# Kernel optimization log

Hardware: AMD Instinct MI355X
Metric: run time of the kernel (lower is better)

The kernel has to match this reference:

```python
import jax, jax.numpy as jnp
import numpy as np
from jax import lax

DIM = 512; NUM_HEADS = 8; WS = 2; POOL = 3
HEAD_DIM = DIM // NUM_HEADS
L_HEADS = int(NUM_HEADS * 0.5); L_DIM = L_HEADS * HEAD_DIM
H_HEADS = NUM_HEADS - L_HEADS; H_DIM = H_HEADS * HEAD_DIM
SCALE = HEAD_DIM ** (-0.5)


def setup_inputs():
    key = jax.random.key(0)
    ks = jax.random.split(key, 8)
    B, Hh, Ww = 8, 64, 64
    N = Hh * Ww
    s = lambda fan: 1.0 / np.sqrt(fan)
    return {
        'x': jax.random.normal(ks[0], (B, N, DIM), jnp.float32),
        'H': Hh,
        'l_q_w': jax.random.normal(ks[1], (DIM, L_DIM), jnp.float32) * s(DIM),
        'l_kv_w': jax.random.normal(ks[2], (DIM, 2 * L_DIM), jnp.float32) * s(DIM),
        'l_proj_w': jax.random.normal(ks[3], (L_DIM, L_DIM), jnp.float32) * s(L_DIM),
        'l_proj_b': jax.random.normal(ks[4], (L_DIM,), jnp.float32) * 0.01,
        'h_qkv_w': jax.random.normal(ks[5], (DIM, H_DIM), jnp.float32) * s(DIM),
        'h_proj_w': jax.random.normal(ks[6], (H_DIM, H_DIM), jnp.float32) * s(H_DIM),
        'h_proj_b': jax.random.normal(ks[7], (H_DIM,), jnp.float32) * 0.01,
    }


def _avgpool3_same(x):
    # x: [M, ws, ws, C]; 3x3 avg pool, stride 1, pad 1, count_include_pad=False
    ssum = lax.reduce_window(x, jnp.float32(0.0), lax.add,
                             (1, POOL, POOL, 1), (1, 1, 1, 1),
                             ((0, 0), (1, 1), (1, 1), (0, 0)))
    ones = jnp.ones(x.shape[1:3], x.dtype)
    cnt = lax.reduce_window(ones, jnp.float32(0.0), lax.add,
                            (POOL, POOL), (1, 1), ((1, 1), (1, 1)))
    return ssum / cnt[None, :, :, None]


def _hifi(x, h_qkv_w, h_proj_w, h_proj_b):
    B, H, W, C = x.shape
    hg, wg = H // WS, W // WS
    x = x @ h_qkv_w  # [B,H,W,H_DIM]
    # partition into ws x ws windows: [B*hg*wg, ws, ws, H_DIM]
    xw = x.reshape(B, hg, WS, wg, WS, H_DIM).transpose(0, 1, 3, 2, 4, 5)
    xw = xw.reshape(B * hg * wg, WS, WS, H_DIM)
    xw = _avgpool3_same(xw) - xw
    xw = xw.reshape(B, hg, wg, WS, WS, H_DIM).transpose(0, 1, 3, 2, 4, 5)
    xw = xw.reshape(B, H, W, H_DIM)
    return xw @ h_proj_w + h_proj_b


def _lofi(x, l_q_w, l_kv_w, l_proj_w, l_proj_b):
    B, H, W, C = x.shape
    q = (x @ l_q_w).reshape(B, H * W, L_HEADS, HEAD_DIM).transpose(0, 2, 1, 3)
    # spatial reduction: avg pool ws stride ws -> [B, H/ws * W/ws, C]
    xp = x.reshape(B, H // WS, WS, W // WS, WS, C).mean(axis=(2, 4))
    xp = xp.reshape(B, -1, C)
    kv = (xp @ l_kv_w).reshape(B, -1, 2, L_HEADS, HEAD_DIM)
    k = kv[:, :, 0].transpose(0, 2, 1, 3)  # [B,h,M,d]
    v = kv[:, :, 1].transpose(0, 2, 1, 3)
    attn = jax.nn.softmax(jnp.einsum('bhnd,bhmd->bhnm', q, k) * SCALE, axis=-1)
    out = jnp.einsum('bhnm,bhmd->bhnd', attn, v)
    out = out.transpose(0, 2, 1, 3).reshape(B, H, W, L_DIM)
    return out @ l_proj_w + l_proj_b


def reference(x, H, l_q_w, l_kv_w, l_proj_w, l_proj_b, h_qkv_w, h_proj_w, h_proj_b):
    B, N, C = x.shape
    W = N // H
    xg = x.reshape(B, H, W, C)
    hi = _hifi(xg, h_qkv_w, h_proj_w, h_proj_b)
    lo = _lofi(xg, l_q_w, l_kv_w, l_proj_w, l_proj_b)
    out = jnp.concatenate([hi, lo], axis=-1)  # [B,H,W,C]
    return out.reshape(B, N, C)
```

## Files before the change

### kernel.cpp

```cpp
#include <hip/hip_runtime.h>

typedef __bf16 bf16x8 __attribute__((ext_vector_type(8)));
typedef float  f32x4  __attribute__((ext_vector_type(4)));
typedef unsigned int u32x4 __attribute__((ext_vector_type(4)));
typedef unsigned short u16x8 __attribute__((ext_vector_type(8)));
typedef unsigned short u16x4 __attribute__((ext_vector_type(4)));
typedef short i16x4 __attribute__((ext_vector_type(4)));

__device__ __forceinline__ unsigned short f2bf(float f) {
    return __builtin_bit_cast(unsigned short, (__bf16)f);
}
__device__ __forceinline__ float bf2f(unsigned short s) {
    return (float)__builtin_bit_cast(__bf16, s);
}
__device__ __forceinline__ bf16x8 as_bf16x8(u32x4 v) {
    return __builtin_bit_cast(bf16x8, v);
}

#define AS1 __attribute__((address_space(1)))
#define AS3 __attribute__((address_space(3)))
__device__ __forceinline__ void gload_lds16(const void* g, void* l) {
    __builtin_amdgcn_global_load_lds((const AS1 void*)g, (AS3 void*)l, 16, 0, 0);
}


__global__ __launch_bounds__(256) void k_prep(
        const float* __restrict__ x,
        const float* __restrict__ h_qkv_w, const float* __restrict__ l_q_w,
        const float* __restrict__ l_kv_w, const float* __restrict__ h_proj_w,
        const float* __restrict__ l_proj_w,
        unsigned short* __restrict__ xb, unsigned short* __restrict__ xpb,
        unsigned short* __restrict__ wcatT, unsigned short* __restrict__ lkvT,
        unsigned short* __restrict__ hprojT, unsigned short* __restrict__ lprojT) {
    int blk = blockIdx.x;
    if (blk < 8192) {
        int t = blk * 256 + threadIdx.x;
        int row = t >> 6, c8 = (t & 63) << 3;
        int b = row >> 12, nn = row & 4095;
        int hh = nn >> 6, ww = nn & 63;
        int mp = (((b << 10) + ((hh >> 1) << 5) + (ww >> 1)) << 2) + ((hh & 1) << 1) + (ww & 1);
        const float* src = x + (size_t)row * 512 + c8;
        f32x4 v0 = *(const f32x4*)src;
        f32x4 v1 = *(const f32x4*)(src + 4);
        u16x8 o = { f2bf(v0[0]), f2bf(v0[1]), f2bf(v0[2]), f2bf(v0[3]),
                    f2bf(v1[0]), f2bf(v1[1]), f2bf(v1[2]), f2bf(v1[3]) };
        *(u16x8*)(xb + (size_t)mp * 512 + c8) = o;
    } else if (blk < 10240) {
        int t = (blk - 8192) * 256 + threadIdx.x;
        int r = t >> 6, c8 = (t & 63) << 3;
        int b = r >> 10, hw = r & 1023;
        int h2 = hw >> 5, w2 = hw & 31;
        const float* base = x + ((size_t)(b << 12) + (h2 << 7) + (w2 << 1)) * 512 + c8;
        u16x8 o;
#pragma unroll
        for (int half = 0; half < 2; half++) {
            f32x4 a0 = *(const f32x4*)(base + half * 4);
            f32x4 a1 = *(const f32x4*)(base + 512 + half * 4);
            f32x4 a2 = *(const f32x4*)(base + 64 * 512 + half * 4);
            f32x4 a3 = *(const f32x4*)(base + 65 * 512 + half * 4);
            f32x4 m = (a0 + a1 + a2 + a3) * 0.25f;
#pragma unroll
            for (int j = 0; j < 4; j++) o[half * 4 + j] = f2bf(m[j]);
        }
        *(u16x8*)(xpb + (size_t)r * 512 + c8) = o;
    } else {
        int i = (blk - 10240) * 256 + threadIdx.x;
        if (i < 262144) {
            int n = i >> 9, k = i & 511;
            float v = (n < 256) ? h_qkv_w[k * 256 + n] : l_q_w[k * 256 + (n - 256)];
            wcatT[i] = f2bf(v);
        } else if (i < 524288) {
            int j = i - 262144; int n = j >> 9, k = j & 511;
            lkvT[j] = f2bf(l_kv_w[k * 512 + n]);
        } else if (i < 589824) {
            int j = i - 524288; int n = j >> 8, k = j & 255;
            hprojT[j] = f2bf(h_proj_w[k * 256 + n]);
        } else {
            int j = i - 589824; int n = j >> 8, k = j & 255;
            lprojT[j] = f2bf(l_proj_w[k * 256 + n]);
        }
    }
}

__device__ __forceinline__ void mm_core(
        const unsigned short* __restrict__ A, const unsigned short* __restrict__ Bt,
        size_t row0, int col0, int K,
        unsigned short* As, unsigned short* Bs, f32x4 (&acc)[4][4]) {
    const int tid = threadIdx.x;
    const int wave = tid >> 6, lane = tid & 63;
    const int m16 = lane & 15, quad = lane >> 4;
    const int wr = wave >> 1, wc = wave & 1;
    const int srow = lane >> 2;
    const int scol = (lane & 3) * 8;
    const unsigned short* Ap0 = A + (row0 + wave * 32 + srow) * (size_t)K + scol;
    const unsigned short* Ap1 = Ap0 + (size_t)16 * K;
    const unsigned short* Bp0 = Bt + (size_t)(col0 + wave * 32 + srow) * K + scol;
    const unsigned short* Bp1 = Bp0 + (size_t)16 * K;
    unsigned short* Al0 = As + wave * 1024;
    unsigned short* Al1 = As + wave * 1024 + 512;
    unsigned short* Bl0 = Bs + wave * 1024;
    unsigned short* Bl1 = Bs + wave * 1024 + 512;

    for (int k0 = 0; k0 < K; k0 += 32) {
        __syncthreads();
        gload_lds16(Ap0 + k0, Al0);
        gload_lds16(Ap1 + k0, Al1);
        gload_lds16(Bp0 + k0, Bl0);
        gload_lds16(Bp1 + k0, Bl1);
        __syncthreads();
        bf16x8 af[4], bfr[4];
#pragma unroll
        for (int mi = 0; mi < 4; mi++)
            af[mi] = as_bf16x8(*(const u32x4*)(As + (wr * 64 + mi * 16 + m16) * 32 + quad * 8));
#pragma unroll
        for (int ni = 0; ni < 4; ni++)
            bfr[ni] = as_bf16x8(*(const u32x4*)(Bs + (wc * 64 + ni * 16 + m16) * 32 + quad * 8));
#pragma unroll
        for (int mi = 0; mi < 4; mi++)
#pragma unroll
            for (int ni = 0; ni < 4; ni++)
                acc[mi][ni] = __builtin_amdgcn_mfma_f32_16x16x32_bf16(af[mi], bfr[ni], acc[mi][ni], 0, 0, 0);
    }
}

__global__ __launch_bounds__(256, 2) void k_mm512(
        const unsigned short* __restrict__ xb, const unsigned short* __restrict__ xpb,
        const unsigned short* __restrict__ wcatT, const unsigned short* __restrict__ lkvT,
        unsigned short* __restrict__ dbuf, unsigned short* __restrict__ qbuf,
        unsigned short* __restrict__ kbuf, unsigned short* __restrict__ vT) {
    __shared__ __align__(16) unsigned short As[128 * 32];
    __shared__ __align__(16) unsigned short Bs[128 * 32];
    const int flat = blockIdx.x;
    const bool isg1 = flat < 1024;
    const unsigned short* A;
    const unsigned short* Bt;
    size_t row0; int col0;
    if (isg1) { A = xb;  Bt = wcatT; row0 = (size_t)(flat >> 2) * 128; col0 = (flat & 3) * 128; }
    else { int f = flat - 1024; A = xpb; Bt = lkvT; row0 = (size_t)(f >> 2) * 128; col0 = (f & 3) * 128; }

    f32x4 acc[4][4] = {};
    mm_core(A, Bt, row0, col0, 512, As, Bs, acc);

    const int tid = threadIdx.x;
    const int wave = tid >> 6, lane = tid & 63;
    const int m16 = lane & 15, quad = lane >> 4;
    const int wr = wave >> 1, wc = wave & 1;

    if (isg1) {
        if (col0 < 256) {
#pragma unroll
            for (int mi = 0; mi < 4; mi++)
#pragma unroll
                for (int ni = 0; ni < 4; ni++) {
                    const int col = col0 + wc * 64 + ni * 16 + m16;
                    const size_t mb = row0 + wr * 64 + mi * 16 + quad * 4;
                    float v0 = acc[mi][ni][0], v1 = acc[mi][ni][1];
                    float v2 = acc[mi][ni][2], v3 = acc[mi][ni][3];
                    float m = 0.25f * ((v0 + v1) + (v2 + v3));
                    dbuf[(mb + 0) * 256 + col] = f2bf(m - v0);
                    dbuf[(mb + 1) * 256 + col] = f2bf(m - v1);
                    dbuf[(mb + 2) * 256 + col] = f2bf(m - v2);
                    dbuf[(mb + 3) * 256 + col] = f2bf(m - v3);
                }
        } else {
#pragma unroll
            for (int mi = 0; mi < 4; mi++)
#pragma unroll
                for (int ni = 0; ni < 4; ni++) {
                    const int col = col0 - 256 + wc * 64 + ni * 16 + m16;
                    const size_t mb = row0 + wr * 64 + mi * 16 + quad * 4;
#pragma unroll
                    for (int r = 0; r < 4; r++)
                        qbuf[(mb + r) * 256 + col] = f2bf(acc[mi][ni][r]);
                }
        }
    } else {
        if (col0 < 256) {
#pragma unroll
            for (int mi = 0; mi < 4; mi++)
#pragma unroll
                for (int ni = 0; ni < 4; ni++) {
                    const int col = col0 + wc * 64 + ni * 16 + m16;
                    const size_t row = row0 + wr * 64 + mi * 16 + quad * 4;
#pragma unroll
                    for (int r = 0; r < 4; r++)
                        kbuf[(row + r) * 256 + col] = f2bf(acc[mi][ni][r]);
                }
        } else {
#pragma unroll
            for (int mi = 0; mi < 4; mi++)
#pragma unroll
                for (int ni = 0; ni < 4; ni++) {
                    const int d = col0 - 256 + wc * 64 + ni * 16 + m16;
                    const int hh = d >> 6, dd = d & 63;
                    const size_t kvg = row0 + wr * 64 + mi * 16 + quad * 4;
                    const int b = (int)(kvg >> 10), kv = (int)(kvg & 1023);
                    u16x4 pk = { f2bf(acc[mi][ni][0]), f2bf(acc[mi][ni][1]),
                                 f2bf(acc[mi][ni][2]), f2bf(acc[mi][ni][3]) };
                    *(u16x4*)(vT + (((size_t)(b * 4 + hh) * 64 + dd) << 10) + kv) = pk;
                }
        }
    }
}

__global__ __launch_bounds__(256, 2) void k_mmproj(
        const unsigned short* __restrict__ dbuf, const unsigned short* __restrict__ aout,
        const unsigned short* __restrict__ hprojT, const unsigned short* __restrict__ lprojT,
        const float* __restrict__ h_proj_b, const float* __restrict__ l_proj_b,
        float* __restrict__ out) {
    __shared__ __align__(16) unsigned short As[128 * 32];
    __shared__ __align__(16) unsigned short Bs[128 * 32];
    const int flat = blockIdx.x;
    const bool hi = flat < 512;
    const int f = flat & 511;
    const unsigned short* A  = hi ? dbuf : aout;
    const unsigned short* Bt = hi ? hprojT : lprojT;
    const float* bias = hi ? h_proj_b : l_proj_b;
    const int coloff = hi ? 0 : 256;
    const size_t row0 = (size_t)(f >> 1) * 128;
    const int col0 = (f & 1) * 128;

    f32x4 acc[4][4] = {};
    mm_core(A, Bt, row0, col0, 256, As, Bs, acc);

    const int tid = threadIdx.x;
    const int wave = tid >> 6, lane = tid & 63;
    const int m16 = lane & 15, quad = lane >> 4;
    const int wr = wave >> 1, wc = wave & 1;

#pragma unroll
    for (int mi = 0; mi < 4; mi++)
#pragma unroll
        for (int ni = 0; ni < 4; ni++) {
            const int col = col0 + wc * 64 + ni * 16 + m16;
            const float bv = bias[col];
            const size_t mb = row0 + wr * 64 + mi * 16 + quad * 4;
            const int widx = (int)(mb >> 2);
            const int b = widx >> 10, rem = widx & 1023;
            const int h2 = rem >> 5, w2 = rem & 31;
            const size_t nb = ((size_t)b << 12) + (h2 << 7) + (w2 << 1);
            float* op = out + nb * 512 + coloff + col;
            op[0]            = acc[mi][ni][0] + bv;
            op[512]          = acc[mi][ni][1] + bv;
            op[64 * 512]     = acc[mi][ni][2] + bv;
            op[65 * 512]     = acc[mi][ni][3] + bv;
        }
}

__global__ __launch_bounds__(256, 2) void k_attn(
        const unsigned short* __restrict__ qbuf,
        const unsigned short* __restrict__ kbuf,
        const unsigned short* __restrict__ vT,
        unsigned short* __restrict__ aout) {
    __shared__ __align__(16) unsigned short Kb[2][64 * 72];
    __shared__ __align__(16) unsigned short Vb[2][64 * 72];
    const int tid = threadIdx.x;
    const int wave = tid >> 6, lane = tid & 63;
    const int m16 = lane & 15, quad = lane >> 4;
    const int qtile = blockIdx.x, bh = blockIdx.y;
    const int b = bh >> 2, h = bh & 3;

    bf16x8 qf[4][2];
    const size_t qrow0 = (size_t)b * 4096 + qtile * 256 + wave * 64;
#pragma unroll
    for (int qh = 0; qh < 4; qh++) {
        const unsigned short* qp = qbuf + (qrow0 + qh * 16 + m16) * 256 + h * 64 + quad * 8;
        qf[qh][0] = as_bf16x8(*(const u32x4*)qp);
        qf[qh][1] = as_bf16x8(*(const u32x4*)(qp + 32));
    }

    f32x4 o[4][4] = {};
    float lp[4] = {0.f, 0.f, 0.f, 0.f};

    const int sr = tid >> 3;
    const int sc = tid & 7;
    const unsigned short* kg = kbuf + ((size_t)b * 1024) * 256 + h * 64 + sc * 8;
    const unsigned short* vg = vT + ((size_t)bh * 64) * 1024 + sc * 8;

    u32x4 s0 = *(const u32x4*)(kg + (size_t)sr * 256);
    u32x4 s1 = *(const u32x4*)(kg + (size_t)(sr + 32) * 256);
    u32x4 s2 = *(const u32x4*)(vg + (size_t)sr * 1024);
    u32x4 s3 = *(const u32x4*)(vg + (size_t)(sr + 32) * 1024);
    *(u32x4*)&Kb[0][sr * 72 + sc * 8] = s0;
    *(u32x4*)&Kb[0][(sr + 32) * 72 + sc * 8] = s1;
    *(u32x4*)&Vb[0][sr * 72 + sc * 8] = s2;
    *(u32x4*)&Vb[0][(sr + 32) * 72 + sc * 8] = s3;

    for (int it = 0; it < 16; ++it) {
        const int cur = it & 1, nxt = cur ^ 1;
        __syncthreads();
        if (it + 1 < 16) {
            const size_t kvb = (size_t)(it + 1) * 64;
            s0 = *(const u32x4*)(kg + (kvb + sr) * 256);
            s1 = *(const u32x4*)(kg + (kvb + sr + 32) * 256);
            s2 = *(const u32x4*)(vg + kvb + (size_t)sr * 1024);
            s3 = *(const u32x4*)(vg + kvb + (size_t)(sr + 32) * 1024);
        }

#pragma unroll
        for (int mt = 0; mt < 4; mt++) {
            const unsigned short* kp = &Kb[cur][(mt * 16 + m16) * 72 + quad * 8];
            const bf16x8 kf0 = as_bf16x8(*(const u32x4*)kp);
            const bf16x8 kf1 = as_bf16x8(*(const u32x4*)(kp + 32));
            f32x4 st[4];
#pragma unroll
            for (int qh = 0; qh < 4; qh++) {
                f32x4 z = {};
                z = __builtin_amdgcn_mfma_f32_16x16x32_bf16(kf0, qf[qh][0], z, 0, 0, 0);
                st[qh] = __builtin_amdgcn_mfma_f32_16x16x32_bf16(kf1, qf[qh][1], z, 0, 0, 0);
            }
            i16x4 pa[4];
#pragma unroll
            for (int qh = 0; qh < 4; qh++) {
                float p0 = __expf(st[qh][0] * 0.125f);
                float p1 = __expf(st[qh][1] * 0.125f);
                float p2 = __expf(st[qh][2] * 0.125f);
                float p3 = __expf(st[qh][3] * 0.125f);
                lp[qh] += (p0 + p1) + (p2 + p3);
                u16x4 pk = { f2bf(p0), f2bf(p1), f2bf(p2), f2bf(p3) };
                pa[qh] = __builtin_bit_cast(i16x4, pk);
            }
#pragma unroll
            for (int nt = 0; nt < 4; nt++) {
                const i16x4 vb = *(const i16x4*)&Vb[cur][(nt * 16 + m16) * 72 + mt * 16 + quad * 4];
#pragma unroll
                for (int qh = 0; qh < 4; qh++)
                    o[qh][nt] = __builtin_amdgcn_mfma_f32_16x16x16bf16_1k(pa[qh], vb, o[qh][nt], 0, 0, 0);
            }
        }

        if (it + 1 < 16) {
            *(u32x4*)&Kb[nxt][sr * 72 + sc * 8] = s0;
            *(u32x4*)&Kb[nxt][(sr + 32) * 72 + sc * 8] = s1;
            *(u32x4*)&Vb[nxt][sr * 72 + sc * 8] = s2;
            *(u32x4*)&Vb[nxt][(sr + 32) * 72 + sc * 8] = s3;
        }
    }

#pragma unroll
    for (int qh = 0; qh < 4; qh++) {
        float l = lp[qh];
        l += __shfl_xor(l, 16);
        l += __shfl_xor(l, 32);
        f32x4 linv;
#pragma unroll
        for (int r = 0; r < 4; r++)
            linv[r] = __builtin_amdgcn_rcpf(__shfl(l, quad * 4 + r));
#pragma unroll
        for (int nt = 0; nt < 4; nt++)
#pragma unroll
            for (int r = 0; r < 4; r++)
                aout[(qrow0 + qh * 16 + quad * 4 + r) * 256 + h * 64 + nt * 16 + m16] =
                    f2bf(o[qh][nt][r] * linv[r]);
    }
}


extern "C" void kernel_launch(void* const* d_in, const int* in_sizes, int n_in,
                              void* d_out, int out_size, void* d_ws, size_t ws_size,
                              hipStream_t stream) {
    (void)in_sizes; (void)n_in; (void)out_size; (void)ws_size;
    const float* x        = (const float*)d_in[0];
    const float* l_q_w    = (const float*)d_in[2];
    const float* l_kv_w   = (const float*)d_in[3];
    const float* l_proj_w = (const float*)d_in[4];
    const float* l_proj_b = (const float*)d_in[5];
    const float* h_qkv_w  = (const float*)d_in[6];
    const float* h_proj_w = (const float*)d_in[7];
    const float* h_proj_b = (const float*)d_in[8];
    float* out = (float*)d_out;

    char* ws = (char*)d_ws;
    unsigned short* xb     = (unsigned short*)(ws);
    unsigned short* aout   = (unsigned short*)(ws);
    unsigned short* dbuf   = (unsigned short*)(ws + 33554432);
    unsigned short* qbuf   = (unsigned short*)(ws + 50331648);
    unsigned short* kbuf   = (unsigned short*)(ws + 67108864);
    unsigned short* vT     = (unsigned short*)(ws + 71303168);
    unsigned short* xpb    = (unsigned short*)(ws + 75497472);
    unsigned short* wcatT  = (unsigned short*)(ws + 83886080);
    unsigned short* lkvT   = (unsigned short*)(ws + 84410368);
    unsigned short* hprojT = (unsigned short*)(ws + 84934656);
    unsigned short* lprojT = (unsigned short*)(ws + 85065728);

    k_prep<<<12800, 256, 0, stream>>>(x, h_qkv_w, l_q_w, l_kv_w, h_proj_w, l_proj_w,
                                      xb, xpb, wcatT, lkvT, hprojT, lprojT);
    k_mm512<<<1280, 256, 0, stream>>>(xb, xpb, wcatT, lkvT, dbuf, qbuf, kbuf, vT);
    k_attn<<<dim3(16, 32), 256, 0, stream>>>(qbuf, kbuf, vT, aout);
    k_mmproj<<<1024, 256, 0, stream>>>(dbuf, aout, hprojT, lprojT, h_proj_b, l_proj_b, out);
}
```

Before: 249.1 us.

## Fold softmax scale into Q and split attention across 8 waves

Pre-multiplies Q by scale*log2(e) in the GEMM epilogue so attention uses exp2 without per-element scaling. Doubles attention block size to 512 threads with 32 query rows per wave, halving per-wave accumulators and splitting K/V staging between wave groups. Aims to raise occupancy and latency hiding on a small grid, at the cost of lower K/V fragment reuse per wave.

```diff
diff --git a/kernel.cpp b/kernel.cpp
--- a/kernel.cpp
+++ b/kernel.cpp
@@ -171,7 +171,7 @@
                     const size_t mb = row0 + wr * 64 + mi * 16 + quad * 4;
 #pragma unroll
                     for (int r = 0; r < 4; r++)
-                        qbuf[(mb + r) * 256 + col] = f2bf(acc[mi][ni][r]);
+                        qbuf[(mb + r) * 256 + col] = f2bf(acc[mi][ni][r] * 0.18033688f);
                 }
         }
     } else {
@@ -247,7 +247,7 @@
         }
 }
 
-__global__ __launch_bounds__(256, 2) void k_attn(
+__global__ __launch_bounds__(512, 4) void k_attn(
         const unsigned short* __restrict__ qbuf,
         const unsigned short* __restrict__ kbuf,
         const unsigned short* __restrict__ vT,
@@ -260,41 +260,50 @@
     const int qtile = blockIdx.x, bh = blockIdx.y;
     const int b = bh >> 2, h = bh & 3;
 
-    bf16x8 qf[4][2];
-    const size_t qrow0 = (size_t)b * 4096 + qtile * 256 + wave * 64;
-#pragma unroll
-    for (int qh = 0; qh < 4; qh++) {
+    bf16x8 qf[2][2];
+    const size_t qrow0 = (size_t)b * 4096 + qtile * 256 + wave * 32;
+#pragma unroll
+    for (int qh = 0; qh < 2; qh++) {
         const unsigned short* qp = qbuf + (qrow0 + qh * 16 + m16) * 256 + h * 64 + quad * 8;
         qf[qh][0] = as_bf16x8(*(const u32x4*)qp);
         qf[qh][1] = as_bf16x8(*(const u32x4*)(qp + 32));
     }
 
-    f32x4 o[4][4] = {};
-    float lp[4] = {0.f, 0.f, 0.f, 0.f};
-
-    const int sr = tid >> 3;
-    const int sc = tid & 7;
+    f32x4 o[2][4] = {};
+    float lp[2] = {0.f, 0.f};
+
+    const int sid = tid & 255;
+    const int sr = sid >> 3;
+    const int sc = sid & 7;
+    const bool stV = tid >= 256;
     const unsigned short* kg = kbuf + ((size_t)b * 1024) * 256 + h * 64 + sc * 8;
     const unsigned short* vg = vT + ((size_t)bh * 64) * 1024 + sc * 8;
 
-    u32x4 s0 = *(const u32x4*)(kg + (size_t)sr * 256);
-    u32x4 s1 = *(const u32x4*)(kg + (size_t)(sr + 32) * 256);
-    u32x4 s2 = *(const u32x4*)(vg + (size_t)sr * 1024);
-    u32x4 s3 = *(const u32x4*)(vg + (size_t)(sr + 32) * 1024);
-    *(u32x4*)&Kb[0][sr * 72 + sc * 8] = s0;
-    *(u32x4*)&Kb[0][(sr + 32) * 72 + sc * 8] = s1;
-    *(u32x4*)&Vb[0][sr * 72 + sc * 8] = s2;
-    *(u32x4*)&Vb[0][(sr + 32) * 72 + sc * 8] = s3;
+    u32x4 s0, s1;
+    if (!stV) {
+        s0 = *(const u32x4*)(kg + (size_t)sr * 256);
+        s1 = *(const u32x4*)(kg + (size_t)(sr + 32) * 256);
+        *(u32x4*)&Kb[0][sr * 72 + sc * 8] = s0;
+        *(u32x4*)&Kb[0][(sr + 32) * 72 + sc * 8] = s1;
+    } else {
+        s0 = *(const u32x4*)(vg + (size_t)sr * 1024);
+        s1 = *(const u32x4*)(vg + (size_t)(sr + 32) * 1024);
+        *(u32x4*)&Vb[0][sr * 72 + sc * 8] = s0;
+        *(u32x4*)&Vb[0][(sr + 32) * 72 + sc * 8] = s1;
+    }
 
     for (int it = 0; it < 16; ++it) {
         const int cur = it & 1, nxt = cur ^ 1;
         __syncthreads();
         if (it + 1 < 16) {
             const size_t kvb = (size_t)(it + 1) * 64;
-            s0 = *(const u32x4*)(kg + (kvb + sr) * 256);
-            s1 = *(const u32x4*)(kg + (kvb + sr + 32) * 256);
-            s2 = *(const u32x4*)(vg + kvb + (size_t)sr * 1024);
-            s3 = *(const u32x4*)(vg + kvb + (size_t)(sr + 32) * 1024);
+            if (!stV) {
+                s0 = *(const u32x4*)(kg + (kvb + sr) * 256);
+                s1 = *(const u32x4*)(kg + (kvb + sr + 32) * 256);
+            } else {
+                s0 = *(const u32x4*)(vg + kvb + (size_t)sr * 1024);
+                s1 = *(const u32x4*)(vg + kvb + (size_t)(sr + 32) * 1024);
+            }
         }
 
 #pragma unroll
@@ -302,20 +311,20 @@
             const unsigned short* kp = &Kb[cur][(mt * 16 + m16) * 72 + quad * 8];
             const bf16x8 kf0 = as_bf16x8(*(const u32x4*)kp);
             const bf16x8 kf1 = as_bf16x8(*(const u32x4*)(kp + 32));
-            f32x4 st[4];
-#pragma unroll
-            for (int qh = 0; qh < 4; qh++) {
+            f32x4 st[2];
+#pragma unroll
+            for (int qh = 0; qh < 2; qh++) {
                 f32x4 z = {};
                 z = __builtin_amdgcn_mfma_f32_16x16x32_bf16(kf0, qf[qh][0], z, 0, 0, 0);
                 st[qh] = __builtin_amdgcn_mfma_f32_16x16x32_bf16(kf1, qf[qh][1], z, 0, 0, 0);
             }
-            i16x4 pa[4];
-#pragma unroll
-            for (int qh = 0; qh < 4; qh++) {
-                float p0 = __expf(st[qh][0] * 0.125f);
-                float p1 = __expf(st[qh][1] * 0.125f);
-                float p2 = __expf(st[qh][2] * 0.125f);
-                float p3 = __expf(st[qh][3] * 0.125f);
+            i16x4 pa[2];
+#pragma unroll
+            for (int qh = 0; qh < 2; qh++) {
+                float p0 = __builtin_exp2f(st[qh][0]);
+                float p1 = __builtin_exp2f(st[qh][1]);
+                float p2 = __builtin_exp2f(st[qh][2]);
+                float p3 = __builtin_exp2f(st[qh][3]);
                 lp[qh] += (p0 + p1) + (p2 + p3);
                 u16x4 pk = { f2bf(p0), f2bf(p1), f2bf(p2), f2bf(p3) };
                 pa[qh] = __builtin_bit_cast(i16x4, pk);
@@ -324,21 +333,24 @@
             for (int nt = 0; nt < 4; nt++) {
                 const i16x4 vb = *(const i16x4*)&Vb[cur][(nt * 16 + m16) * 72 + mt * 16 + quad * 4];
 #pragma unroll
-                for (int qh = 0; qh < 4; qh++)
+                for (int qh = 0; qh < 2; qh++)
                     o[qh][nt] = __builtin_amdgcn_mfma_f32_16x16x16bf16_1k(pa[qh], vb, o[qh][nt], 0, 0, 0);
             }
         }
 
         if (it + 1 < 16) {
-            *(u32x4*)&Kb[nxt][sr * 72 + sc * 8] = s0;
-            *(u32x4*)&Kb[nxt][(sr + 32) * 72 + sc * 8] = s1;
-            *(u32x4*)&Vb[nxt][sr * 72 + sc * 8] = s2;
-            *(u32x4*)&Vb[nxt][(sr + 32) * 72 + sc * 8] = s3;
-        }
-    }
-
-#pragma unroll
-    for (int qh = 0; qh < 4; qh++) {
+            if (!stV) {
+                *(u32x4*)&Kb[nxt][sr * 72 + sc * 8] = s0;
+                *(u32x4*)&Kb[nxt][(sr + 32) * 72 + sc * 8] = s1;
+            } else {
+                *(u32x4*)&Vb[nxt][sr * 72 + sc * 8] = s0;
+                *(u32x4*)&Vb[nxt][(sr + 32) * 72 + sc * 8] = s1;
+            }
+        }
+    }
+
+#pragma unroll
+    for (int qh = 0; qh < 2; qh++) {
         float l = lp[qh];
         l += __shfl_xor(l, 16);
         l += __shfl_xor(l, 32);
@@ -386,6 +398,6 @@
     k_prep<<<12800, 256, 0, stream>>>(x, h_qkv_w, l_q_w, l_kv_w, h_proj_w, l_proj_w,
                                       xb, xpb, wcatT, lkvT, hprojT, lprojT);
     k_mm512<<<1280, 256, 0, stream>>>(xb, xpb, wcatT, lkvT, dbuf, qbuf, kbuf, vT);
-    k_attn<<<dim3(16, 32), 256, 0, stream>>>(qbuf, kbuf, vT, aout);
+    k_attn<<<dim3(16, 32), 512, 0, stream>>>(qbuf, kbuf, vT, aout);
     k_mmproj<<<1024, 256, 0, stream>>>(dbuf, aout, hprojT, lprojT, h_proj_b, l_proj_b, out);
 }
```

New measurement: 254.7 us. +2.2%, slower.

## Co-schedule hi-freq projection with attention and fold softmax scale into Q

Applied to the files above, without the earlier changes.

Merges the attention kernel and the hi-frequency output projection into one launch, with blocks branching on their index, so the independent hifi GEMM fills the GPU alongside the 512 attention blocks. The lofi projection becomes its own smaller kernel. Q is pre-scaled by scale*log2(e) when it is written, so the softmax uses exp2 with no per-element multiply. The shared memory array is unified and the kernel requests 4 blocks per CU via launch bounds, which may raise register pressure for the attention branch.

```diff
diff --git a/kernel.cpp b/kernel.cpp
--- a/kernel.cpp
+++ b/kernel.cpp
@@ -171,7 +171,7 @@
                     const size_t mb = row0 + wr * 64 + mi * 16 + quad * 4;
 #pragma unroll
                     for (int r = 0; r < 4; r++)
-                        qbuf[(mb + r) * 256 + col] = f2bf(acc[mi][ni][r]);
+                        qbuf[(mb + r) * 256 + col] = f2bf(acc[mi][ni][r] * 0.18033688f);
                 }
         }
     } else {
@@ -203,25 +203,164 @@
     }
 }
 
-__global__ __launch_bounds__(256, 2) void k_mmproj(
-        const unsigned short* __restrict__ dbuf, const unsigned short* __restrict__ aout,
-        const unsigned short* __restrict__ hprojT, const unsigned short* __restrict__ lprojT,
-        const float* __restrict__ h_proj_b, const float* __restrict__ l_proj_b,
+__global__ __launch_bounds__(256, 4) void k_attn_hiproj(
+        const unsigned short* __restrict__ qbuf,
+        const unsigned short* __restrict__ kbuf,
+        const unsigned short* __restrict__ vT,
+        unsigned short* __restrict__ aout,
+        const unsigned short* __restrict__ dbuf,
+        const unsigned short* __restrict__ hprojT,
+        const float* __restrict__ h_proj_b,
+        float* __restrict__ out) {
+    __shared__ __align__(16) unsigned short smem[4 * 64 * 72];
+    const int bx = blockIdx.x;
+    const int tid = threadIdx.x;
+    const int wave = tid >> 6, lane = tid & 63;
+    const int m16 = lane & 15, quad = lane >> 4;
+
+    if (bx < 512) {
+        unsigned short* Kb = smem;
+        unsigned short* Vb = smem + 2 * 64 * 72;
+        const int qtile = bx & 15, bh = bx >> 4;
+        const int b = bh >> 2, h = bh & 3;
+
+        bf16x8 qf[4][2];
+        const size_t qrow0 = (size_t)b * 4096 + qtile * 256 + wave * 64;
+#pragma unroll
+        for (int qh = 0; qh < 4; qh++) {
+            const unsigned short* qp = qbuf + (qrow0 + qh * 16 + m16) * 256 + h * 64 + quad * 8;
+            qf[qh][0] = as_bf16x8(*(const u32x4*)qp);
+            qf[qh][1] = as_bf16x8(*(const u32x4*)(qp + 32));
+        }
+
+        f32x4 o[4][4] = {};
+        float lp[4] = {0.f, 0.f, 0.f, 0.f};
+
+        const int sr = tid >> 3;
+        const int sc = tid & 7;
+        const unsigned short* kg = kbuf + ((size_t)b * 1024) * 256 + h * 64 + sc * 8;
+        const unsigned short* vg = vT + ((size_t)bh * 64) * 1024 + sc * 8;
+
+        u32x4 s0 = *(const u32x4*)(kg + (size_t)sr * 256);
+        u32x4 s1 = *(const u32x4*)(kg + (size_t)(sr + 32) * 256);
+        u32x4 s2 = *(const u32x4*)(vg + (size_t)sr * 1024);
+        u32x4 s3 = *(const u32x4*)(vg + (size_t)(sr + 32) * 1024);
+        *(u32x4*)&Kb[sr * 72 + sc * 8] = s0;
+        *(u32x4*)&Kb[(sr + 32) * 72 + sc * 8] = s1;
+        *(u32x4*)&Vb[sr * 72 + sc * 8] = s2;
+        *(u32x4*)&Vb[(sr + 32) * 72 + sc * 8] = s3;
+
+        for (int it = 0; it < 16; ++it) {
+            const int cur = (it & 1) * 4608, nxt = cur ^ 4608;
+            __syncthreads();
+            if (it + 1 < 16) {
+                const size_t kvb = (size_t)(it + 1) * 64;
+                s0 = *(const u32x4*)(kg + (kvb + sr) * 256);
+                s1 = *(const u32x4*)(kg + (kvb + sr + 32) * 256);
+                s2 = *(const u32x4*)(vg + kvb + (size_t)sr * 1024);
+                s3 = *(const u32x4*)(vg + kvb + (size_t)(sr + 32) * 1024);
+            }
+
+#pragma unroll
+            for (int mt = 0; mt < 4; mt++) {
+                const unsigned short* kp = &Kb[cur + (mt * 16 + m16) * 72 + quad * 8];
+                const bf16x8 kf0 = as_bf16x8(*(const u32x4*)kp);
+                const bf16x8 kf1 = as_bf16x8(*(const u32x4*)(kp + 32));
+                f32x4 st[4];
+#pragma unroll
+                for (int qh = 0; qh < 4; qh++) {
+                    f32x4 z = {};
+                    z = __builtin_amdgcn_mfma_f32_16x16x32_bf16(kf0, qf[qh][0], z, 0, 0, 0);
+                    st[qh] = __builtin_amdgcn_mfma_f32_16x16x32_bf16(kf1, qf[qh][1], z, 0, 0, 0);
+                }
+                i16x4 pa[4];
+#pragma unroll
+                for (int qh = 0; qh < 4; qh++) {
+                    float p0 = __builtin_exp2f(st[qh][0]);
+                    float p1 = __builtin_exp2f(st[qh][1]);
+                    float p2 = __builtin_exp2f(st[qh][2]);
+                    float p3 = __builtin_exp2f(st[qh][3]);
+                    lp[qh] += (p0 + p1) + (p2 + p3);
+                    u16x4 pk = { f2bf(p0), f2bf(p1), f2bf(p2), f2bf(p3) };
+                    pa[qh] = __builtin_bit_cast(i16x4, pk);
+                }
+#pragma unroll
+                for (int nt = 0; nt < 4; nt++) {
+                    const i16x4 vb = *(const i16x4*)&Vb[cur + (nt * 16 + m16) * 72 + mt * 16 + quad * 4];
+#pragma unroll
+                    for (int qh = 0; qh < 4; qh++)
+                        o[qh][nt] = __builtin_amdgcn_mfma_f32_16x16x16bf16_1k(pa[qh], vb, o[qh][nt], 0, 0, 0);
+                }
+            }
+
+            if (it + 1 < 16) {
+                *(u32x4*)&Kb[nxt + sr * 72 + sc * 8] = s0;
+                *(u32x4*)&Kb[nxt + (sr + 32) * 72 + sc * 8] = s1;
+                *(u32x4*)&Vb[nxt + sr * 72 + sc * 8] = s2;
+                *(u32x4*)&Vb[nxt + (sr + 32) * 72 + sc * 8] = s3;
+            }
+        }
+
+#pragma unroll
+        for (int qh = 0; qh < 4; qh++) {
+            float l = lp[qh];
+            l += __shfl_xor(l, 16);
+            l += __shfl_xor(l, 32);
+            f32x4 linv;
+#pragma unroll
+            for (int r = 0; r < 4; r++)
+                linv[r] = __builtin_amdgcn_rcpf(__shfl(l, quad * 4 + r));
+#pragma unroll
+            for (int nt = 0; nt < 4; nt++)
+#pragma unroll
+                for (int r = 0; r < 4; r++)
+                    aout[(qrow0 + qh * 16 + quad * 4 + r) * 256 + h * 64 + nt * 16 + m16] =
+                        f2bf(o[qh][nt][r] * linv[r]);
+        }
+    } else {
+        unsigned short* As = smem;
+        unsigned short* Bs = smem + 128 * 32;
+        const int f = bx - 512;
+        const size_t row0 = (size_t)(f >> 1) * 128;
+        const int col0 = (f & 1) * 128;
+
+        f32x4 acc[4][4] = {};
+        mm_core(dbuf, hprojT, row0, col0, 256, As, Bs, acc);
+
+        const int wr = wave >> 1, wc = wave & 1;
+#pragma unroll
+        for (int mi = 0; mi < 4; mi++)
+#pragma unroll
+            for (int ni = 0; ni < 4; ni++) {
+                const int col = col0 + wc * 64 + ni * 16 + m16;
+                const float bv = h_proj_b[col];
+                const size_t mb = row0 + wr * 64 + mi * 16 + quad * 4;
+                const int widx = (int)(mb >> 2);
+                const int b = widx >> 10, rem = widx & 1023;
+                const int h2 = rem >> 5, w2 = rem & 31;
+                const size_t nb = ((size_t)b << 12) + (h2 << 7) + (w2 << 1);
+                float* op = out + nb * 512 + col;
+                op[0]            = acc[mi][ni][0] + bv;
+                op[512]          = acc[mi][ni][1] + bv;
+                op[64 * 512]     = acc[mi][ni][2] + bv;
+                op[65 * 512]     = acc[mi][ni][3] + bv;
+            }
+    }
+}
+
+__global__ __launch_bounds__(256, 2) void k_mmproj_lo(
+        const unsigned short* __restrict__ aout,
+        const unsigned short* __restrict__ lprojT,
+        const float* __restrict__ l_proj_b,
         float* __restrict__ out) {
     __shared__ __align__(16) unsigned short As[128 * 32];
     __shared__ __align__(16) unsigned short Bs[128 * 32];
-    const int flat = blockIdx.x;
-    const bool hi = flat < 512;
-    const int f = flat & 511;
-    const unsigned short* A  = hi ? dbuf : aout;
-    const unsigned short* Bt = hi ? hprojT : lprojT;
-    const float* bias = hi ? h_proj_b : l_proj_b;
-    const int coloff = hi ? 0 : 256;
+    const int f = blockIdx.x;
     const size_t row0 = (size_t)(f >> 1) * 128;
     const int col0 = (f & 1) * 128;
 
     f32x4 acc[4][4] = {};
-    mm_core(A, Bt, row0, col0, 256, As, Bs, acc);
+    mm_core(aout, lprojT, row0, col0, 256, As, Bs, acc);
 
     const int tid = threadIdx.x;
     const int wave = tid >> 6, lane = tid & 63;
@@ -233,126 +372,18 @@
 #pragma unroll
         for (int ni = 0; ni < 4; ni++) {
             const int col = col0 + wc * 64 + ni * 16 + m16;
-            const float bv = bias[col];
+            const float bv = l_proj_b[col];
             const size_t mb = row0 + wr * 64 + mi * 16 + quad * 4;
             const int widx = (int)(mb >> 2);
             const int b = widx >> 10, rem = widx & 1023;
             const int h2 = rem >> 5, w2 = rem & 31;
             const size_t nb = ((size_t)b << 12) + (h2 << 7) + (w2 << 1);
-            float* op = out + nb * 512 + coloff + col;
+            float* op = out + nb * 512 + 256 + col;
             op[0]            = acc[mi][ni][0] + bv;
             op[512]          = acc[mi][ni][1] + bv;
             op[64 * 512]     = acc[mi][ni][2] + bv;
             op[65 * 512]     = acc[mi][ni][3] + bv;
         }
-}
-
-__global__ __launch_bounds__(256, 2) void k_attn(
-        const unsigned short* __restrict__ qbuf,
-        const unsigned short* __restrict__ kbuf,
-        const unsigned short* __restrict__ vT,
-        unsigned short* __restrict__ aout) {
-    __shared__ __align__(16) unsigned short Kb[2][64 * 72];
-    __shared__ __align__(16) unsigned short Vb[2][64 * 72];
-    const int tid = threadIdx.x;
-    const int wave = tid >> 6, lane = tid & 63;
-    const int m16 = lane & 15, quad = lane >> 4;
-    const int qtile = blockIdx.x, bh = blockIdx.y;
-    const int b = bh >> 2, h = bh & 3;
-
-    bf16x8 qf[4][2];
-    const size_t qrow0 = (size_t)b * 4096 + qtile * 256 + wave * 64;
-#pragma unroll
-    for (int qh = 0; qh < 4; qh++) {
-        const unsigned short* qp = qbuf + (qrow0 + qh * 16 + m16) * 256 + h * 64 + quad * 8;
-        qf[qh][0] = as_bf16x8(*(const u32x4*)qp);
-        qf[qh][1] = as_bf16x8(*(const u32x4*)(qp + 32));
-    }
-
-    f32x4 o[4][4] = {};
-    float lp[4] = {0.f, 0.f, 0.f, 0.f};
-
-    const int sr = tid >> 3;
-    const int sc = tid & 7;
-    const unsigned short* kg = kbuf + ((size_t)b * 1024) * 256 + h * 64 + sc * 8;
-    const unsigned short* vg = vT + ((size_t)bh * 64) * 1024 + sc * 8;
-
-    u32x4 s0 = *(const u32x4*)(kg + (size_t)sr * 256);
-    u32x4 s1 = *(const u32x4*)(kg + (size_t)(sr + 32) * 256);
-    u32x4 s2 = *(const u32x4*)(vg + (size_t)sr * 1024);
-    u32x4 s3 = *(const u32x4*)(vg + (size_t)(sr + 32) * 1024);
-    *(u32x4*)&Kb[0][sr * 72 + sc * 8] = s0;
-    *(u32x4*)&Kb[0][(sr + 32) * 72 + sc * 8] = s1;
-    *(u32x4*)&Vb[0][sr * 72 + sc * 8] = s2;
-    *(u32x4*)&Vb[0][(sr + 32) * 72 + sc * 8] = s3;
-
-    for (int it = 0; it < 16; ++it) {
-        const int cur = it & 1, nxt = cur ^ 1;
-        __syncthreads();
-        if (it + 1 < 16) {
-            const size_t kvb = (size_t)(it + 1) * 64;
-            s0 = *(const u32x4*)(kg + (kvb + sr) * 256);
-            s1 = *(const u32x4*)(kg + (kvb + sr + 32) * 256);
-            s2 = *(const u32x4*)(vg + kvb + (size_t)sr * 1024);
-            s3 = *(const u32x4*)(vg + kvb + (size_t)(sr + 32) * 1024);
-        }
-
-#pragma unroll
-        for (int mt = 0; mt < 4; mt++) {
-            const unsigned short* kp = &Kb[cur][(mt * 16 + m16) * 72 + quad * 8];
-            const bf16x8 kf0 = as_bf16x8(*(const u32x4*)kp);
-            const bf16x8 kf1 = as_bf16x8(*(const u32x4*)(kp + 32));
-            f32x4 st[4];
-#pragma unroll
-            for (int qh = 0; qh < 4; qh++) {
-                f32x4 z = {};
-                z = __builtin_amdgcn_mfma_f32_16x16x32_bf16(kf0, qf[qh][0], z, 0, 0, 0);
-                st[qh] = __builtin_amdgcn_mfma_f32_16x16x32_bf16(kf1, qf[qh][1], z, 0, 0, 0);
-            }
-            i16x4 pa[4];
-#pragma unroll
-            for (int qh = 0; qh < 4; qh++) {
-                float p0 = __expf(st[qh][0] * 0.125f);
-                float p1 = __expf(st[qh][1] * 0.125f);
-                float p2 = __expf(st[qh][2] * 0.125f);
-                float p3 = __expf(st[qh][3] * 0.125f);
-                lp[qh] += (p0 + p1) + (p2 + p3);
-                u16x4 pk = { f2bf(p0), f2bf(p1), f2bf(p2), f2bf(p3) };
-                pa[qh] = __builtin_bit_cast(i16x4, pk);
-            }
-#pragma unroll
-            for (int nt = 0; nt < 4; nt++) {
-                const i16x4 vb = *(const i16x4*)&Vb[cur][(nt * 16 + m16) * 72 + mt * 16 + quad * 4];
-#pragma unroll
-                for (int qh = 0; qh < 4; qh++)
-                    o[qh][nt] = __builtin_amdgcn_mfma_f32_16x16x16bf16_1k(pa[qh], vb, o[qh][nt], 0, 0, 0);
-            }
-        }
-
-        if (it + 1 < 16) {
-            *(u32x4*)&Kb[nxt][sr * 72 + sc * 8] = s0;
-            *(u32x4*)&Kb[nxt][(sr + 32) * 72 + sc * 8] = s1;
-            *(u32x4*)&Vb[nxt][sr * 72 + sc * 8] = s2;
-            *(u32x4*)&Vb[nxt][(sr + 32) * 72 + sc * 8] = s3;
-        }
-    }
-
-#pragma unroll
-    for (int qh = 0; qh < 4; qh++) {
-        float l = lp[qh];
-        l += __shfl_xor(l, 16);
-        l += __shfl_xor(l, 32);
-        f32x4 linv;
-#pragma unroll
-        for (int r = 0; r < 4; r++)
-            linv[r] = __builtin_amdgcn_rcpf(__shfl(l, quad * 4 + r));
-#pragma unroll
-        for (int nt = 0; nt < 4; nt++)
-#pragma unroll
-            for (int r = 0; r < 4; r++)
-                aout[(qrow0 + qh * 16 + quad * 4 + r) * 256 + h * 64 + nt * 16 + m16] =
-                    f2bf(o[qh][nt][r] * linv[r]);
-    }
 }
 
 
@@ -386,6 +417,6 @@
     k_prep<<<12800, 256, 0, stream>>>(x, h_qkv_w, l_q_w, l_kv_w, h_proj_w, l_proj_w,
                                       xb, xpb, wcatT, lkvT, hprojT, lprojT);
     k_mm512<<<1280, 256, 0, stream>>>(xb, xpb, wcatT, lkvT, dbuf, qbuf, kbuf, vT);
-    k_attn<<<dim3(16, 32), 256, 0, stream>>>(qbuf, kbuf, vT, aout);
-    k_mmproj<<<1024, 256, 0, stream>>>(dbuf, aout, hprojT, lprojT, h_proj_b, l_proj_b, out);
-}
+    k_attn_hiproj<<<1024, 256, 0, stream>>>(qbuf, kbuf, vT, aout, dbuf, hprojT, h_proj_b, out);
+    k_mmproj_lo<<<512, 256, 0, stream>>>(aout, lprojT, l_proj_b, out);
+}
```

Measured after the change: 561.9 us. 126% more time.

## Split attention KV range across two wave groups, fuse pooling into prep, fold scale into Q

Applied to the files above, without the earlier changes.

The attention kernel now runs 512 threads per block. Two groups of four waves each process half of the key/value sequence and combine their partial outputs and row sums through shared memory before normalising. This doubles the number of waves in flight for the 512-block grid. The prep kernel reads each 2x2 window of x once and writes both the bf16 copy and the pooled row, removing a second pass over x. The softmax scale times log2(e) is folded into Q at GEMM epilogue time so the attention can use exp2 directly, at the cost of one extra rounding on Q.

```diff
diff --git a/kernel.cpp b/kernel.cpp
--- a/kernel.cpp
+++ b/kernel.cpp
@@ -9,9 +9,6 @@
 
 __device__ __forceinline__ unsigned short f2bf(float f) {
     return __builtin_bit_cast(unsigned short, (__bf16)f);
-}
-__device__ __forceinline__ float bf2f(unsigned short s) {
-    return (float)__builtin_bit_cast(__bf16, s);
 }
 __device__ __forceinline__ bf16x8 as_bf16x8(u32x4 v) {
     return __builtin_bit_cast(bf16x8, v);
@@ -33,38 +30,30 @@
         unsigned short* __restrict__ wcatT, unsigned short* __restrict__ lkvT,
         unsigned short* __restrict__ hprojT, unsigned short* __restrict__ lprojT) {
     int blk = blockIdx.x;
-    if (blk < 8192) {
+    if (blk < 2048) {
         int t = blk * 256 + threadIdx.x;
-        int row = t >> 6, c8 = (t & 63) << 3;
-        int b = row >> 12, nn = row & 4095;
-        int hh = nn >> 6, ww = nn & 63;
-        int mp = (((b << 10) + ((hh >> 1) << 5) + (ww >> 1)) << 2) + ((hh & 1) << 1) + (ww & 1);
-        const float* src = x + (size_t)row * 512 + c8;
-        f32x4 v0 = *(const f32x4*)src;
-        f32x4 v1 = *(const f32x4*)(src + 4);
-        u16x8 o = { f2bf(v0[0]), f2bf(v0[1]), f2bf(v0[2]), f2bf(v0[3]),
-                    f2bf(v1[0]), f2bf(v1[1]), f2bf(v1[2]), f2bf(v1[3]) };
-        *(u16x8*)(xb + (size_t)mp * 512 + c8) = o;
-    } else if (blk < 10240) {
-        int t = (blk - 8192) * 256 + threadIdx.x;
-        int r = t >> 6, c8 = (t & 63) << 3;
-        int b = r >> 10, hw = r & 1023;
-        int h2 = hw >> 5, w2 = hw & 31;
+        int widx = t >> 6, c8 = (t & 63) << 3;
+        int b = widx >> 10, rem = widx & 1023;
+        int h2 = rem >> 5, w2 = rem & 31;
         const float* base = x + ((size_t)(b << 12) + (h2 << 7) + (w2 << 1)) * 512 + c8;
-        u16x8 o;
-#pragma unroll
-        for (int half = 0; half < 2; half++) {
-            f32x4 a0 = *(const f32x4*)(base + half * 4);
-            f32x4 a1 = *(const f32x4*)(base + 512 + half * 4);
-            f32x4 a2 = *(const f32x4*)(base + 64 * 512 + half * 4);
-            f32x4 a3 = *(const f32x4*)(base + 65 * 512 + half * 4);
-            f32x4 m = (a0 + a1 + a2 + a3) * 0.25f;
-#pragma unroll
-            for (int j = 0; j < 4; j++) o[half * 4 + j] = f2bf(m[j]);
-        }
-        *(u16x8*)(xpb + (size_t)r * 512 + c8) = o;
+        f32x4 acc0 = {}, acc1 = {};
+        const int roff[4] = {0, 1, 64, 65};
+#pragma unroll
+        for (int j = 0; j < 4; j++) {
+            const float* src = base + (size_t)roff[j] * 512;
+            f32x4 v0 = *(const f32x4*)src;
+            f32x4 v1 = *(const f32x4*)(src + 4);
+            acc0 += v0; acc1 += v1;
+            u16x8 o = { f2bf(v0[0]), f2bf(v0[1]), f2bf(v0[2]), f2bf(v0[3]),
+                        f2bf(v1[0]), f2bf(v1[1]), f2bf(v1[2]), f2bf(v1[3]) };
+            *(u16x8*)(xb + ((size_t)widx * 4 + j) * 512 + c8) = o;
+        }
+        acc0 *= 0.25f; acc1 *= 0.25f;
+        u16x8 p = { f2bf(acc0[0]), f2bf(acc0[1]), f2bf(acc0[2]), f2bf(acc0[3]),
+                    f2bf(acc1[0]), f2bf(acc1[1]), f2bf(acc1[2]), f2bf(acc1[3]) };
+        *(u16x8*)(xpb + (size_t)widx * 512 + c8) = p;
     } else {
-        int i = (blk - 10240) * 256 + threadIdx.x;
+        int i = (blk - 2048) * 256 + threadIdx.x;
         if (i < 262144) {
             int n = i >> 9, k = i & 511;
             float v = (n < 256) ? h_qkv_w[k * 256 + n] : l_q_w[k * 256 + (n - 256)];
@@ -171,7 +160,7 @@
                     const size_t mb = row0 + wr * 64 + mi * 16 + quad * 4;
 #pragma unroll
                     for (int r = 0; r < 4; r++)
-                        qbuf[(mb + r) * 256 + col] = f2bf(acc[mi][ni][r]);
+                        qbuf[(mb + r) * 256 + col] = f2bf(acc[mi][ni][r] * 0.18033688f);
                 }
         }
     } else {
@@ -247,21 +236,21 @@
         }
 }
 
-__global__ __launch_bounds__(256, 2) void k_attn(
+__global__ __launch_bounds__(512, 4) void k_attn(
         const unsigned short* __restrict__ qbuf,
         const unsigned short* __restrict__ kbuf,
         const unsigned short* __restrict__ vT,
         unsigned short* __restrict__ aout) {
-    __shared__ __align__(16) unsigned short Kb[2][64 * 72];
-    __shared__ __align__(16) unsigned short Vb[2][64 * 72];
+    __shared__ __align__(16) unsigned short smem[36864];
     const int tid = threadIdx.x;
     const int wave = tid >> 6, lane = tid & 63;
+    const int half = wave >> 2, qw = wave & 3;
     const int m16 = lane & 15, quad = lane >> 4;
     const int qtile = blockIdx.x, bh = blockIdx.y;
     const int b = bh >> 2, h = bh & 3;
 
     bf16x8 qf[4][2];
-    const size_t qrow0 = (size_t)b * 4096 + qtile * 256 + wave * 64;
+    const size_t qrow0 = (size_t)b * 4096 + qtile * 256 + qw * 64;
 #pragma unroll
     for (int qh = 0; qh < 4; qh++) {
         const unsigned short* qp = qbuf + (qrow0 + qh * 16 + m16) * 256 + h * 64 + quad * 8;
@@ -272,24 +261,28 @@
     f32x4 o[4][4] = {};
     float lp[4] = {0.f, 0.f, 0.f, 0.f};
 
-    const int sr = tid >> 3;
-    const int sc = tid & 7;
-    const unsigned short* kg = kbuf + ((size_t)b * 1024) * 256 + h * 64 + sc * 8;
-    const unsigned short* vg = vT + ((size_t)bh * 64) * 1024 + sc * 8;
+    const int sid = tid & 255;
+    const int sr = sid >> 3;
+    const int sc = sid & 7;
+    const size_t kvoff = (size_t)half * 512;
+    const unsigned short* kg = kbuf + ((size_t)b * 1024 + kvoff) * 256 + h * 64 + sc * 8;
+    const unsigned short* vg = vT + ((size_t)bh * 64) * 1024 + kvoff + sc * 8;
+    unsigned short* Kh = smem + half * 2 * 4608;
+    unsigned short* Vh = smem + 18432 + half * 2 * 4608;
 
     u32x4 s0 = *(const u32x4*)(kg + (size_t)sr * 256);
     u32x4 s1 = *(const u32x4*)(kg + (size_t)(sr + 32) * 256);
     u32x4 s2 = *(const u32x4*)(vg + (size_t)sr * 1024);
     u32x4 s3 = *(const u32x4*)(vg + (size_t)(sr + 32) * 1024);
-    *(u32x4*)&Kb[0][sr * 72 + sc * 8] = s0;
-    *(u32x4*)&Kb[0][(sr + 32) * 72 + sc * 8] = s1;
-    *(u32x4*)&Vb[0][sr * 72 + sc * 8] = s2;
-    *(u32x4*)&Vb[0][(sr + 32) * 72 + sc * 8] = s3;
-
-    for (int it = 0; it < 16; ++it) {
-        const int cur = it & 1, nxt = cur ^ 1;
+    *(u32x4*)&Kh[sr * 72 + sc * 8] = s0;
+    *(u32x4*)&Kh[(sr + 32) * 72 + sc * 8] = s1;
+    *(u32x4*)&Vh[sr * 72 + sc * 8] = s2;
+    *(u32x4*)&Vh[(sr + 32) * 72 + sc * 8] = s3;
+
+    for (int it = 0; it < 8; ++it) {
+        const int cur = (it & 1) * 4608, nxt = cur ^ 4608;
         __syncthreads();
-        if (it + 1 < 16) {
+        if (it + 1 < 8) {
             const size_t kvb = (size_t)(it + 1) * 64;
             s0 = *(const u32x4*)(kg + (kvb + sr) * 256);
             s1 = *(const u32x4*)(kg + (kvb + sr + 32) * 256);
@@ -299,7 +292,7 @@
 
 #pragma unroll
         for (int mt = 0; mt < 4; mt++) {
-            const unsigned short* kp = &Kb[cur][(mt * 16 + m16) * 72 + quad * 8];
+            const unsigned short* kp = &Kh[cur + (mt * 16 + m16) * 72 + quad * 8];
             const bf16x8 kf0 = as_bf16x8(*(const u32x4*)kp);
             const bf16x8 kf1 = as_bf16x8(*(const u32x4*)(kp + 32));
             f32x4 st[4];
@@ -312,46 +305,69 @@
             i16x4 pa[4];
 #pragma unroll
             for (int qh = 0; qh < 4; qh++) {
-                float p0 = __expf(st[qh][0] * 0.125f);
-                float p1 = __expf(st[qh][1] * 0.125f);
-                float p2 = __expf(st[qh][2] * 0.125f);
-                float p3 = __expf(st[qh][3] * 0.125f);
+                float p0 = __builtin_exp2f(st[qh][0]);
+                float p1 = __builtin_exp2f(st[qh][1]);
+                float p2 = __builtin_exp2f(st[qh][2]);
+                float p3 = __builtin_exp2f(st[qh][3]);
                 lp[qh] += (p0 + p1) + (p2 + p3);
                 u16x4 pk = { f2bf(p0), f2bf(p1), f2bf(p2), f2bf(p3) };
                 pa[qh] = __builtin_bit_cast(i16x4, pk);
             }
 #pragma unroll
             for (int nt = 0; nt < 4; nt++) {
-                const i16x4 vb = *(const i16x4*)&Vb[cur][(nt * 16 + m16) * 72 + mt * 16 + quad * 4];
+                const i16x4 vb = *(const i16x4*)&Vh[cur + (nt * 16 + m16) * 72 + mt * 16 + quad * 4];
 #pragma unroll
                 for (int qh = 0; qh < 4; qh++)
                     o[qh][nt] = __builtin_amdgcn_mfma_f32_16x16x16bf16_1k(pa[qh], vb, o[qh][nt], 0, 0, 0);
             }
         }
 
-        if (it + 1 < 16) {
-            *(u32x4*)&Kb[nxt][sr * 72 + sc * 8] = s0;
-            *(u32x4*)&Kb[nxt][(sr + 32) * 72 + sc * 8] = s1;
-            *(u32x4*)&Vb[nxt][sr * 72 + sc * 8] = s2;
-            *(u32x4*)&Vb[nxt][(sr + 32) * 72 + sc * 8] = s3;
-        }
-    }
-
-#pragma unroll
-    for (int qh = 0; qh < 4; qh++) {
-        float l = lp[qh];
-        l += __shfl_xor(l, 16);
-        l += __shfl_xor(l, 32);
-        f32x4 linv;
-#pragma unroll
-        for (int r = 0; r < 4; r++)
-            linv[r] = __builtin_amdgcn_rcpf(__shfl(l, quad * 4 + r));
-#pragma unroll
-        for (int nt = 0; nt < 4; nt++)
+        if (it + 1 < 8) {
+            *(u32x4*)&Kh[nxt + sr * 72 + sc * 8] = s0;
+            *(u32x4*)&Kh[nxt + (sr + 32) * 72 + sc * 8] = s1;
+            *(u32x4*)&Vh[nxt + sr * 72 + sc * 8] = s2;
+            *(u32x4*)&Vh[nxt + (sr + 32) * 72 + sc * 8] = s3;
+        }
+    }
+
+    __syncthreads();
+    float* scratch = (float*)smem;
+    float* wbase = scratch + qw * 4352;
+    if (half == 1) {
+#pragma unroll
+        for (int qh = 0; qh < 4; qh++)
+#pragma unroll
+            for (int nt = 0; nt < 4; nt++)
+                *(f32x4*)&wbase[((qh * 4 + nt) * 64 + lane) * 4] = o[qh][nt];
+#pragma unroll
+        for (int qh = 0; qh < 4; qh++)
+            wbase[4096 + qh * 64 + lane] = lp[qh];
+    }
+    __syncthreads();
+    if (half == 0) {
+#pragma unroll
+        for (int qh = 0; qh < 4; qh++) {
+#pragma unroll
+            for (int nt = 0; nt < 4; nt++)
+                o[qh][nt] += *(const f32x4*)&wbase[((qh * 4 + nt) * 64 + lane) * 4];
+            lp[qh] += wbase[4096 + qh * 64 + lane];
+        }
+#pragma unroll
+        for (int qh = 0; qh < 4; qh++) {
+            float l = lp[qh];
+            l += __shfl_xor(l, 16);
+            l += __shfl_xor(l, 32);
+            f32x4 linv;
 #pragma unroll
             for (int r = 0; r < 4; r++)
-                aout[(qrow0 + qh * 16 + quad * 4 + r) * 256 + h * 64 + nt * 16 + m16] =
-                    f2bf(o[qh][nt][r] * linv[r]);
+                linv[r] = __builtin_amdgcn_rcpf(__shfl(l, quad * 4 + r));
+#pragma unroll
+            for (int nt = 0; nt < 4; nt++)
+#pragma unroll
+                for (int r = 0; r < 4; r++)
+                    aout[(qrow0 + qh * 16 + quad * 4 + r) * 256 + h * 64 + nt * 16 + m16] =
+                        f2bf(o[qh][nt][r] * linv[r]);
+        }
     }
 }
 
@@ -383,9 +399,9 @@
     unsigned short* hprojT = (unsigned short*)(ws + 84934656);
     unsigned short* lprojT = (unsigned short*)(ws + 85065728);
 
-    k_prep<<<12800, 256, 0, stream>>>(x, h_qkv_w, l_q_w, l_kv_w, h_proj_w, l_proj_w,
-                                      xb, xpb, wcatT, lkvT, hprojT, lprojT);
+    k_prep<<<4608, 256, 0, stream>>>(x, h_qkv_w, l_q_w, l_kv_w, h_proj_w, l_proj_w,
+                                     xb, xpb, wcatT, lkvT, hprojT, lprojT);
     k_mm512<<<1280, 256, 0, stream>>>(xb, xpb, wcatT, lkvT, dbuf, qbuf, kbuf, vT);
-    k_attn<<<dim3(16, 32), 256, 0, stream>>>(qbuf, kbuf, vT, aout);
+    k_attn<<<dim3(16, 32), 512, 0, stream>>>(qbuf, kbuf, vT, aout);
     k_mmproj<<<1024, 256, 0, stream>>>(dbuf, aout, hprojT, lprojT, h_proj_b, l_proj_b, out);
 }
```

Measured after the change: 500.3 us. 101% more time.
